# Performance work log

Hardware: AMD Instinct MI355X
Metric: run time of the kernel (lower is better)

## Reference

```python
import jax, jax.numpy as jnp
import numpy as np

N = 100000      # nodes
E = 800000      # directed edges
D_IN = 128      # input features (n_inputs)
HIDDEN = 128    # conf['model']['hidden_size']
D_OUT = 2       # conv2 output classes


def setup_inputs() -> dict:
    key = jax.random.key(0)
    k0, k1, k2, k3 = jax.random.split(key, 4)
    x = jax.random.normal(k0, (N, D_IN), dtype=jnp.float32)
    edge_index = jax.random.randint(k1, (2, E), 0, N, dtype=jnp.int32)
    # Glorot-style init for GCNConv weights, zero bias (PyG defaults)
    s1 = float(np.sqrt(6.0 / (D_IN + HIDDEN)))
    s2 = float(np.sqrt(6.0 / (HIDDEN + D_OUT)))
    W1 = jax.random.uniform(k2, (D_IN, HIDDEN), jnp.float32, -s1, s1)
    b1 = jnp.zeros((HIDDEN,), jnp.float32)
    W2 = jax.random.uniform(k3, (HIDDEN, D_OUT), jnp.float32, -s2, s2)
    b2 = jnp.zeros((D_OUT,), jnp.float32)
    return {"x": x, "edge_index": edge_index, "W1": W1, "b1": b1, "W2": W2, "b2": b2}


def gcn_conv(x, src, dst, W, b):
    """PyG GCNConv: add self-loops, symmetric deg^-1/2 A deg^-1/2 normalization."""
    n = x.shape[0]
    h = x @ W                                                   # [N, F_out]
    ones_e = jnp.ones((src.shape[0],), h.dtype)
    # degree with self-loops (init to 1)
    deg = jnp.ones((n,), h.dtype).at[dst].add(ones_e)           # [N]
    dinv = 1.0 / jnp.sqrt(deg)
    norm = (dinv[src] * dinv[dst])[:, None]                     # [E, 1]
    # self-loop contribution: norm_ii = dinv_i^2; then scatter edge messages
    out = (h * (dinv * dinv)[:, None]).at[dst].add(h[src] * norm)
    return out + b


def reference(x, edge_index, W1, b1, W2, b2):
    src, dst = edge_index[0], edge_index[1]
    h = jax.nn.relu(gcn_conv(x, src, dst, W1, b1))
    return gcn_conv(h, src, dst, W2, b2)                        # [N, 2]
```

## Files before the change

kernel.cpp:

```cpp
#include <hip/hip_runtime.h>
#include <hip/hip_bf16.h>


#define D1 128
#define BSH 9
#define BSZ (1 << BSH)
#define CHA 4096

typedef __attribute__((ext_vector_type(8))) short short8;
typedef __attribute__((ext_vector_type(4))) float floatx4;

__device__ __forceinline__ unsigned short f2bf(float f) {
    unsigned u = __float_as_uint(f);
    u += 0x7fff + ((u >> 16) & 1);
    return (unsigned short)(u >> 16);
}
__device__ __forceinline__ float bflo(unsigned u) { return __uint_as_float(u << 16); }
__device__ __forceinline__ float bfhi(unsigned u) { return __uint_as_float(u & 0xffff0000u); }

__global__ void k_init(const float* __restrict__ W1, unsigned short* __restrict__ W1t,
                       int* __restrict__ bcount) {
    int i = blockIdx.x * 256 + threadIdx.x;
    if (i < 256) bcount[i] = 0;
    if (i < D1 * D1) {
        int c = i >> 7, k = i & 127;
        W1t[c * D1 + k] = f2bf(W1[k * D1 + c]);
    }
}

__global__ __launch_bounds__(256) void k_bcount(const int* __restrict__ dst,
                                                int* __restrict__ bcount,
                                                int E, int nbuck) {
    __shared__ int h[256];
    int t = threadIdx.x;
    h[t] = 0;
    __syncthreads();
    for (int i = blockIdx.x * 256 + t; i < E; i += gridDim.x * 256)
        atomicAdd(&h[dst[i] >> BSH], 1);
    __syncthreads();
    if (t < nbuck && h[t]) atomicAdd(&bcount[t], h[t]);
}

__global__ __launch_bounds__(256) void k_bscan(const int* __restrict__ bcount,
                                               int* __restrict__ bbase,
                                               int* __restrict__ bcur,
                                               int* __restrict__ rowptr,
                                               int nbuck, int N, int E) {
    __shared__ int sd[256];
    int t = threadIdx.x;
    int v = (t < nbuck) ? bcount[t] : 0;
    sd[t] = v;
    __syncthreads();
    for (int off = 1; off < 256; off <<= 1) {
        int x = (t >= off) ? sd[t - off] : 0;
        __syncthreads();
        sd[t] += x;
        __syncthreads();
    }
    int excl = sd[t] - v;
    if (t <= nbuck) bbase[t] = (t < nbuck) ? excl : E;
    if (t < nbuck) bcur[t] = excl;
    if (t == 0) {
        bbase[nbuck] = E;
        rowptr[N] = E;
    }
}

__global__ __launch_bounds__(256) void k_binA(
    const int* __restrict__ src, const int* __restrict__ dst,
    int* __restrict__ bcur, unsigned* __restrict__ packed, int E, int nbuck)
{
    __shared__ int hist[256];
    __shared__ int cur[256];
    const int t = threadIdx.x;
    const int e0 = blockIdx.x * CHA;
    const int e1 = min(e0 + CHA, E);

    for (int i = t; i < nbuck; i += 256) hist[i] = 0;
    __syncthreads();
    for (int i = e0 + t; i < e1; i += 256)
        atomicAdd(&hist[dst[i] >> BSH], 1);
    __syncthreads();
    for (int i = t; i < nbuck; i += 256)
        cur[i] = (hist[i] > 0) ? atomicAdd(&bcur[i], hist[i]) : 0;
    __syncthreads();
    for (int i = e0 + t; i < e1; i += 256) {
        int d = dst[i];
        int b = d >> BSH;
        int pos = atomicAdd(&cur[b], 1);
        packed[pos] = ((unsigned)src[i] << BSH) | (unsigned)(d & (BSZ - 1));
    }
}

__global__ __launch_bounds__(512) void k_binB(
    const int* __restrict__ bbase, const unsigned* __restrict__ packed,
    int* __restrict__ rowptr, float* __restrict__ dinv,
    int* __restrict__ esrc, int* __restrict__ order, int N)
{
    __shared__ int lh[BSZ];
    __shared__ int sd[BSZ];
    __shared__ int lcur[BSZ];
    __shared__ int dbin[64];
    __shared__ int dcur[64];

    const int t = threadIdx.x;
    const int s = blockIdx.x << BSH;
    const int n = min(BSZ, N - s);
    const int base = bbase[blockIdx.x];
    const int cnt = bbase[blockIdx.x + 1] - base;

    lh[t] = 0;
    if (t < 64) dbin[t] = 0;
    __syncthreads();
    for (int i = t; i < cnt; i += 512)
        atomicAdd(&lh[packed[base + i] & (BSZ - 1)], 1);
    __syncthreads();

    sd[t] = lh[t];
    __syncthreads();
    for (int off = 1; off < BSZ; off <<= 1) {
        int x = (t >= off) ? sd[t - off] : 0;
        __syncthreads();
        sd[t] += x;
        __syncthreads();
    }
    int excl = sd[t] - lh[t];
    if (t < n) {
        rowptr[s + t] = base + excl;
        dinv[s + t] = rsqrtf(1.0f + (float)lh[t]);
        atomicAdd(&dbin[min(lh[t], 63)], 1);
    }
    lcur[t] = excl;
    __syncthreads();

    for (int i = t; i < cnt; i += 512) {
        unsigned p = packed[base + i];
        int ld = (int)(p & (BSZ - 1));
        int pos = atomicAdd(&lcur[ld], 1);
        esrc[base + pos] = (int)(p >> BSH);
    }

    __syncthreads();
    if (t < 64) sd[t] = dbin[t];
    __syncthreads();
    for (int off = 1; off < 64; off <<= 1) {
        int x = (t >= off && t < 64) ? sd[t - off] : 0;
        __syncthreads();
        if (t < 64) sd[t] += x;
        __syncthreads();
    }
    if (t < 64) dcur[t] = sd[t] - dbin[t];
    __syncthreads();
    if (t < n) {
        int b = min(lh[t], 63);
        int pos = atomicAdd(&dcur[b], 1);
        order[s + pos] = s + t;
    }
}

#define BMM 64
__global__ __launch_bounds__(256) void k_gemm1(
    const float* __restrict__ x, const unsigned short* __restrict__ W1t,
    const float* __restrict__ dinv, unsigned short* __restrict__ h1s, int N)
{
    __shared__ unsigned short Xs[BMM][136];
    __shared__ unsigned short Ws[D1][136];

    const int t = threadIdx.x;
    const int row0 = blockIdx.x * BMM;

#pragma unroll
    for (int i = 0; i < 8; ++i) {
        int idx = t + 256 * i;
        int r = idx >> 4, c8 = idx & 15;
        short8 v = ((const short8*)W1t)[r * 16 + c8];
        *(short8*)&Ws[r][c8 * 8] = v;
    }
#pragma unroll
    for (int i = 0; i < 4; ++i) {
        int idx = t + 256 * i;
        int r = idx >> 4, c8 = idx & 15;
        int row = row0 + r;
        short8 v8 = (short8)0;
        if (row < N) {
            const float* p = x + (size_t)row * D1 + c8 * 8;
            float4 f0 = *(const float4*)p;
            float4 f1 = *(const float4*)(p + 4);
            v8[0] = (short)f2bf(f0.x); v8[1] = (short)f2bf(f0.y);
            v8[2] = (short)f2bf(f0.z); v8[3] = (short)f2bf(f0.w);
            v8[4] = (short)f2bf(f1.x); v8[5] = (short)f2bf(f1.y);
            v8[6] = (short)f2bf(f1.z); v8[7] = (short)f2bf(f1.w);
        }
        *(short8*)&Xs[r][c8 * 8] = v8;
    }
    __syncthreads();

    const int w = t >> 6;
    const int l = t & 63;
    const int m = l & 15;
    const int q = l >> 4;

    floatx4 acc[8];
#pragma unroll
    for (int c = 0; c < 8; ++c) acc[c] = (floatx4)0.0f;

#pragma unroll
    for (int ks = 0; ks < 4; ++ks) {
        short8 a = *(const short8*)&Xs[16 * w + m][ks * 32 + q * 8];
#pragma unroll
        for (int c = 0; c < 8; ++c) {
            short8 b = *(const short8*)&Ws[c * 16 + m][ks * 32 + q * 8];
            acc[c] = __builtin_amdgcn_mfma_f32_16x16x32_bf16(a, b, acc[c], 0, 0, 0);
        }
    }

#pragma unroll
    for (int r = 0; r < 4; ++r) {
        int row = row0 + 16 * w + q * 4 + r;
        if (row >= N) continue;
        float di = dinv[row];
#pragma unroll
        for (int c = 0; c < 8; ++c)
            h1s[(size_t)row * D1 + c * 16 + m] = f2bf(acc[c][r] * di);
    }
}

__global__ __launch_bounds__(256) void k_agg1_gemm2(
    const int* __restrict__ rowptr, const int* __restrict__ esrc,
    const int* __restrict__ order,
    const float* __restrict__ dinv, const unsigned short* __restrict__ h1s,
    const float* __restrict__ b1, const float* __restrict__ W2,
    float* __restrict__ h2s, int N)
{
    int gid = blockIdx.x * 256 + threadIdx.x;
    int grp = gid >> 4;
    if (grp >= N) return;
    int node = order[grp];
    int lane = gid & 15;

    const uint4* h1v = (const uint4*)h1s;

    uint4 u = h1v[(size_t)node * 16 + lane];
    float accA[8], accB[8];
    accA[0] = bflo(u.x); accA[1] = bfhi(u.x);
    accA[2] = bflo(u.y); accA[3] = bfhi(u.y);
    accA[4] = bflo(u.z); accA[5] = bfhi(u.z);
    accA[6] = bflo(u.w); accA[7] = bfhi(u.w);
#pragma unroll
    for (int j = 0; j < 8; ++j) accB[j] = 0.f;

    int beg = rowptr[node], end = rowptr[node + 1];
    int e = beg;
    for (; e + 3 < end; e += 4) {
        int s0 = esrc[e], s1 = esrc[e + 1], s2 = esrc[e + 2], s3 = esrc[e + 3];
        uint4 v0 = h1v[(size_t)s0 * 16 + lane];
        uint4 v1 = h1v[(size_t)s1 * 16 + lane];
        uint4 v2 = h1v[(size_t)s2 * 16 + lane];
        uint4 v3 = h1v[(size_t)s3 * 16 + lane];
        accA[0] += bflo(v0.x); accA[1] += bfhi(v0.x);
        accA[2] += bflo(v0.y); accA[3] += bfhi(v0.y);
        accA[4] += bflo(v0.z); accA[5] += bfhi(v0.z);
        accA[6] += bflo(v0.w); accA[7] += bfhi(v0.w);
        accB[0] += bflo(v1.x); accB[1] += bfhi(v1.x);
        accB[2] += bflo(v1.y); accB[3] += bfhi(v1.y);
        accB[4] += bflo(v1.z); accB[5] += bfhi(v1.z);
        accB[6] += bflo(v1.w); accB[7] += bfhi(v1.w);
        accA[0] += bflo(v2.x); accA[1] += bfhi(v2.x);
        accA[2] += bflo(v2.y); accA[3] += bfhi(v2.y);
        accA[4] += bflo(v2.z); accA[5] += bfhi(v2.z);
        accA[6] += bflo(v2.w); accA[7] += bfhi(v2.w);
        accB[0] += bflo(v3.x); accB[1] += bfhi(v3.x);
        accB[2] += bflo(v3.y); accB[3] += bfhi(v3.y);
        accB[4] += bflo(v3.z); accB[5] += bfhi(v3.z);
        accB[6] += bflo(v3.w); accB[7] += bfhi(v3.w);
    }
    for (; e < end; ++e) {
        uint4 v = h1v[(size_t)esrc[e] * 16 + lane];
        accB[0] += bflo(v.x); accB[1] += bfhi(v.x);
        accB[2] += bflo(v.y); accB[3] += bfhi(v.y);
        accB[4] += bflo(v.z); accB[5] += bfhi(v.z);
        accB[6] += bflo(v.w); accB[7] += bfhi(v.w);
    }

    float di = dinv[node];
    const float4* b1v = (const float4*)b1;
    float4 bbA = b1v[lane * 2 + 0];
    float4 bbB = b1v[lane * 2 + 1];
    float a[8];
    a[0] = fmaxf((accA[0] + accB[0]) * di + bbA.x, 0.f);
    a[1] = fmaxf((accA[1] + accB[1]) * di + bbA.y, 0.f);
    a[2] = fmaxf((accA[2] + accB[2]) * di + bbA.z, 0.f);
    a[3] = fmaxf((accA[3] + accB[3]) * di + bbA.w, 0.f);
    a[4] = fmaxf((accA[4] + accB[4]) * di + bbB.x, 0.f);
    a[5] = fmaxf((accA[5] + accB[5]) * di + bbB.y, 0.f);
    a[6] = fmaxf((accA[6] + accB[6]) * di + bbB.z, 0.f);
    a[7] = fmaxf((accA[7] + accB[7]) * di + bbB.w, 0.f);

    const float4* W2v = (const float4*)W2;
    float p0 = 0.f, p1 = 0.f;
#pragma unroll
    for (int j2 = 0; j2 < 4; ++j2) {
        float4 wv = W2v[lane * 4 + j2];
        p0 += a[j2 * 2] * wv.x + a[j2 * 2 + 1] * wv.z;
        p1 += a[j2 * 2] * wv.y + a[j2 * 2 + 1] * wv.w;
    }

#pragma unroll
    for (int off = 8; off > 0; off >>= 1) {
        p0 += __shfl_xor(p0, off);
        p1 += __shfl_xor(p1, off);
    }
    if (lane == 0) {
        h2s[(size_t)node * 2 + 0] = p0 * di;
        h2s[(size_t)node * 2 + 1] = p1 * di;
    }
}

__global__ void k_gather2(const int* __restrict__ rowptr, const int* __restrict__ esrc,
                          const float* __restrict__ h2s, const float* __restrict__ dinv,
                          const float* __restrict__ b2, float* __restrict__ out, int N)
{
    int i = blockIdx.x * 256 + threadIdx.x;
    if (i >= N) return;
    const float2* h2v = (const float2*)h2s;
    float2 h = h2v[i];
    float o0a = h.x, o1a = h.y;
    float o0b = 0.f, o1b = 0.f;
    int beg = rowptr[i], end = rowptr[i + 1];
    int e = beg;
    for (; e + 3 < end; e += 4) {
        int s0 = esrc[e], s1 = esrc[e + 1], s2 = esrc[e + 2], s3 = esrc[e + 3];
        float2 v0 = h2v[s0];
        float2 v1 = h2v[s1];
        float2 v2 = h2v[s2];
        float2 v3 = h2v[s3];
        o0a += v0.x + v2.x; o1a += v0.y + v2.y;
        o0b += v1.x + v3.x; o1b += v1.y + v3.y;
    }
    for (; e < end; ++e) {
        float2 v = h2v[esrc[e]];
        o0b += v.x; o1b += v.y;
    }
    float di = dinv[i];
    ((float2*)out)[i] = make_float2((o0a + o0b) * di + b2[0], (o1a + o1b) * di + b2[1]);
}

extern "C" void kernel_launch(void* const* d_in, const int* in_sizes, int n_in,
                              void* d_out, int out_size, void* d_ws, size_t ws_size,
                              hipStream_t stream)
{
    const float* x  = (const float*)d_in[0];
    const int*   ei = (const int*)d_in[1];
    const float* W1 = (const float*)d_in[2];
    const float* b1 = (const float*)d_in[3];
    const float* W2 = (const float*)d_in[4];
    const float* b2 = (const float*)d_in[5];
    float* out = (float*)d_out;

    const int N = in_sizes[0] / D1;
    const int E = in_sizes[1] / 2;
    const int* src = ei;
    const int* dst = ei + E;

    char* w = (char*)d_ws;
    auto alloc = [&](size_t bytes) -> char* {
        char* r = w;
        w += (bytes + 15) & ~(size_t)15;
        return r;
    };
    unsigned short* h1s = (unsigned short*)alloc((size_t)N * D1 * 2);
    unsigned short* W1t = (unsigned short*)alloc((size_t)D1 * D1 * 2);
    float* h2s    = (float*)alloc((size_t)N * 2 * 4);
    float* dinv   = (float*)alloc((size_t)N * 4);
    int*   rowptr = (int*)alloc((size_t)(N + 4) * 4);
    int*   order  = (int*)alloc((size_t)N * 4);
    int*   bcount = (int*)alloc(256 * 4);
    int*   bbase  = (int*)alloc(260 * 4);
    int*   bcur   = (int*)alloc(256 * 4);
    unsigned* packed = (unsigned*)alloc((size_t)E * 4);
    int*   esrc   = (int*)alloc((size_t)E * 4);

    const int nbuck = (N + BSZ - 1) >> BSH;

    k_init  <<<(D1 * D1 + 255) / 256, 256, 0, stream>>>(W1, W1t, bcount);
    k_bcount<<<256, 256, 0, stream>>>(dst, bcount, E, nbuck);
    k_bscan <<<1, 256, 0, stream>>>(bcount, bbase, bcur, rowptr, nbuck, N, E);
    k_binA  <<<(E + CHA - 1) / CHA, 256, 0, stream>>>(src, dst, bcur, packed, E, nbuck);
    k_binB  <<<nbuck, 512, 0, stream>>>(bbase, packed, rowptr, dinv, esrc, order, N);

    k_gemm1<<<(N + BMM - 1) / BMM, 256, 0, stream>>>(x, W1t, dinv, h1s, N);

    k_agg1_gemm2<<<(N * 16 + 255) / 256, 256, 0, stream>>>(rowptr, esrc, order, dinv, h1s, b1, W2, h2s, N);

    k_gather2<<<(N + 255) / 256, 256, 0, stream>>>(rowptr, esrc, h2s, dinv, b2, out, N);
}
```

Baseline: 199.1 us.

## Slice h1 into feature-major chunks so aggregation gathers stay cache-resident

The layer-1 GEMM now writes h1 as 8 feature slices of 16 bf16 columns, each stored contiguously over all nodes. The aggregation kernel is split so each block handles one slice for 128 nodes with 2 threads per node. The goal is a smaller per-slice working set (about 3.2 MB) for the random neighbour gathers, which should improve L2/MALL hit rates. The cost is partial W2 products written to a new buffer and an extra reduction kernel, plus edge indices being re-read once per slice. A small cleanup in the bucket scan drops a redundant store.

```diff
diff --git a/kernel.cpp b/kernel.cpp
--- a/kernel.cpp
+++ b/kernel.cpp
@@ -58,8 +58,7 @@
         __syncthreads();
     }
     int excl = sd[t] - v;
-    if (t <= nbuck) bbase[t] = (t < nbuck) ? excl : E;
-    if (t < nbuck) bcur[t] = excl;
+    if (t < nbuck) { bbase[t] = excl; bcur[t] = excl; }
     if (t == 0) {
         bbase[nbuck] = E;
         rowptr[N] = E;
@@ -221,26 +220,28 @@
         float di = dinv[row];
 #pragma unroll
         for (int c = 0; c < 8; ++c)
-            h1s[(size_t)row * D1 + c * 16 + m] = f2bf(acc[c][r] * di);
-    }
-}
-
-__global__ __launch_bounds__(256) void k_agg1_gemm2(
+            h1s[((size_t)c * N + row) * 16 + m] = f2bf(acc[c][r] * di);
+    }
+}
+
+__global__ __launch_bounds__(256) void k_agg1(
     const int* __restrict__ rowptr, const int* __restrict__ esrc,
-    const int* __restrict__ order,
-    const float* __restrict__ dinv, const unsigned short* __restrict__ h1s,
+    const int* __restrict__ order, const float* __restrict__ dinv,
+    const unsigned short* __restrict__ h1s,
     const float* __restrict__ b1, const float* __restrict__ W2,
-    float* __restrict__ h2s, int N)
-{
-    int gid = blockIdx.x * 256 + threadIdx.x;
-    int grp = gid >> 4;
+    float2* __restrict__ hp, int N)
+{
+    const int slice = blockIdx.x & 7;
+    const int chunk = blockIdx.x >> 3;
+    const int t = threadIdx.x;
+    const int grp = chunk * 128 + (t >> 1);
     if (grp >= N) return;
-    int node = order[grp];
-    int lane = gid & 15;
-
-    const uint4* h1v = (const uint4*)h1s;
-
-    uint4 u = h1v[(size_t)node * 16 + lane];
+    const int half = t & 1;
+    const int node = order[grp];
+
+    const uint4* hv = (const uint4*)h1s + (size_t)slice * N * 2;
+
+    uint4 u = hv[(size_t)node * 2 + half];
     float accA[8], accB[8];
     accA[0] = bflo(u.x); accA[1] = bfhi(u.x);
     accA[2] = bflo(u.y); accA[3] = bfhi(u.y);
@@ -253,10 +254,10 @@
     int e = beg;
     for (; e + 3 < end; e += 4) {
         int s0 = esrc[e], s1 = esrc[e + 1], s2 = esrc[e + 2], s3 = esrc[e + 3];
-        uint4 v0 = h1v[(size_t)s0 * 16 + lane];
-        uint4 v1 = h1v[(size_t)s1 * 16 + lane];
-        uint4 v2 = h1v[(size_t)s2 * 16 + lane];
-        uint4 v3 = h1v[(size_t)s3 * 16 + lane];
+        uint4 v0 = hv[(size_t)s0 * 2 + half];
+        uint4 v1 = hv[(size_t)s1 * 2 + half];
+        uint4 v2 = hv[(size_t)s2 * 2 + half];
+        uint4 v3 = hv[(size_t)s3 * 2 + half];
         accA[0] += bflo(v0.x); accA[1] += bfhi(v0.x);
         accA[2] += bflo(v0.y); accA[3] += bfhi(v0.y);
         accA[4] += bflo(v0.z); accA[5] += bfhi(v0.z);
@@ -275,7 +276,7 @@
         accB[6] += bflo(v3.w); accB[7] += bfhi(v3.w);
     }
     for (; e < end; ++e) {
-        uint4 v = h1v[(size_t)esrc[e] * 16 + lane];
+        uint4 v = hv[(size_t)esrc[e] * 2 + half];
         accB[0] += bflo(v.x); accB[1] += bfhi(v.x);
         accB[2] += bflo(v.y); accB[3] += bfhi(v.y);
         accB[4] += bflo(v.z); accB[5] += bfhi(v.z);
@@ -283,9 +284,10 @@
     }
 
     float di = dinv[node];
+    const int f0 = slice * 16 + half * 8;
     const float4* b1v = (const float4*)b1;
-    float4 bbA = b1v[lane * 2 + 0];
-    float4 bbB = b1v[lane * 2 + 1];
+    float4 bbA = b1v[f0 >> 2];
+    float4 bbB = b1v[(f0 >> 2) + 1];
     float a[8];
     a[0] = fmaxf((accA[0] + accB[0]) * di + bbA.x, 0.f);
     a[1] = fmaxf((accA[1] + accB[1]) * di + bbA.y, 0.f);
@@ -300,20 +302,29 @@
     float p0 = 0.f, p1 = 0.f;
 #pragma unroll
     for (int j2 = 0; j2 < 4; ++j2) {
-        float4 wv = W2v[lane * 4 + j2];
+        float4 wv = W2v[(f0 >> 1) + j2];
         p0 += a[j2 * 2] * wv.x + a[j2 * 2 + 1] * wv.z;
         p1 += a[j2 * 2] * wv.y + a[j2 * 2 + 1] * wv.w;
     }
-
-#pragma unroll
-    for (int off = 8; off > 0; off >>= 1) {
-        p0 += __shfl_xor(p0, off);
-        p1 += __shfl_xor(p1, off);
-    }
-    if (lane == 0) {
-        h2s[(size_t)node * 2 + 0] = p0 * di;
-        h2s[(size_t)node * 2 + 1] = p1 * di;
-    }
+    p0 += __shfl_xor(p0, 1);
+    p1 += __shfl_xor(p1, 1);
+    if (half == 0) hp[(size_t)slice * N + grp] = make_float2(p0, p1);
+}
+
+__global__ void k_h2red(const float2* __restrict__ hp, const int* __restrict__ order,
+                        const float* __restrict__ dinv, float* __restrict__ h2s, int N)
+{
+    int g = blockIdx.x * 256 + threadIdx.x;
+    if (g >= N) return;
+    float p0 = 0.f, p1 = 0.f;
+#pragma unroll
+    for (int s = 0; s < 8; ++s) {
+        float2 v = hp[(size_t)s * N + g];
+        p0 += v.x; p1 += v.y;
+    }
+    int node = order[g];
+    float di = dinv[node];
+    ((float2*)h2s)[node] = make_float2(p0 * di, p1 * di);
 }
 
 __global__ void k_gather2(const int* __restrict__ rowptr, const int* __restrict__ esrc,
@@ -371,6 +382,7 @@
     unsigned short* h1s = (unsigned short*)alloc((size_t)N * D1 * 2);
     unsigned short* W1t = (unsigned short*)alloc((size_t)D1 * D1 * 2);
     float* h2s    = (float*)alloc((size_t)N * 2 * 4);
+    float2* hp    = (float2*)alloc((size_t)N * 8 * 8);
     float* dinv   = (float*)alloc((size_t)N * 4);
     int*   rowptr = (int*)alloc((size_t)(N + 4) * 4);
     int*   order  = (int*)alloc((size_t)N * 4);
@@ -390,7 +402,9 @@
 
     k_gemm1<<<(N + BMM - 1) / BMM, 256, 0, stream>>>(x, W1t, dinv, h1s, N);
 
-    k_agg1_gemm2<<<(N * 16 + 255) / 256, 256, 0, stream>>>(rowptr, esrc, order, dinv, h1s, b1, W2, h2s, N);
+    const int nchunk = (N + 127) / 128;
+    k_agg1 <<<nchunk * 8, 256, 0, stream>>>(rowptr, esrc, order, dinv, h1s, b1, W2, hp, N);
+    k_h2red<<<(N + 255) / 256, 256, 0, stream>>>(hp, order, dinv, h2s, N);
 
     k_gather2<<<(N + 255) / 256, 256, 0, stream>>>(rowptr, esrc, h2s, dinv, b2, out, N);
 }
```

Result: slower. 227.0 us (+14.0%).
